# Performance work log

Hardware: AMD Instinct MI355X
Metric: run time of the kernel (lower is better)

The kernel has to match this reference:

```python
import jax, jax.numpy as jnp
import numpy as np

V = 8192        # num_embeddings == n_nodes
E = 262144      # n_edges (avg degree 32)
N = 262144      # lookup batch
D = 128         # out_channels
LAMDA = 0.8
EPS = 1e-12


def setup_inputs() -> dict:
    key = jax.random.key(0)
    k0, k1, k2, k3, k4 = jax.random.split(key, 5)
    x = jax.random.randint(k0, (N,), 0, V)
    edge_index = jax.random.randint(k1, (2, E), 0, V)
    edge_weight = jax.random.uniform(k2, (E,), dtype=jnp.float32)
    embedding = jax.random.normal(k3, (V, V), dtype=jnp.float32) * 0.02
    W = jax.random.normal(k4, (V, D), dtype=jnp.float32) * (1.0 / np.sqrt(V))
    b = jnp.zeros((D,), dtype=jnp.float32)
    return {"x": x, "edge_index": edge_index, "edge_weight": edge_weight,
            "embedding": embedding, "W": W, "b": b}


def reference(x, edge_index, edge_weight, embedding, W, b):
    # Embedding_sim: linear transform then sparse adjacency propagation
    H = embedding @ W + b                       # [V, D]
    src, dst = edge_index[0], edge_index[1]
    msg = H[src] * edge_weight[:, None]         # gather + weight, [E, D]
    P = jax.ops.segment_sum(msg, dst, num_segments=V)  # spmm(A, H), [V, D]
    emb = LAMDA * P + (1.0 - LAMDA) * H         # [V, D]
    # dropout is identity in eval mode
    out = emb[x]                                # embedding lookup, [N, D]
    norm = jnp.linalg.norm(out, axis=-1, keepdims=True)
    return out / jnp.maximum(norm, EPS)         # F.normalize (L2, dim=1)
```

## Files before the change

kernel.cpp:

```cpp
#include <hip/hip_runtime.h>
#include <hip/hip_bf16.h>

#define V     8192
#define E_N   262144
#define NN    262144
#define D     128
#define KDIM  8192

typedef __attribute__((ext_vector_type(8))) short b16x8;
typedef __attribute__((ext_vector_type(8))) unsigned short u16x8;
typedef __attribute__((ext_vector_type(4))) float f32x4;
typedef __attribute__((ext_vector_type(4))) unsigned int u32x4;

static __device__ __forceinline__ unsigned short f2bf(float f) {
    union { float f; unsigned int u; } v; v.f = f;
    unsigned int r = v.u + 0x7FFFu + ((v.u >> 16) & 1u);
    return (unsigned short)(r >> 16);
}

__global__ void k_wbt(const float* __restrict__ W, unsigned short* __restrict__ WbT) {
    __shared__ float tile[32][33];
    int bk = blockIdx.x & 255;
    int bn = blockIdx.x >> 8;
    int r = threadIdx.x >> 5;
    int c = threadIdx.x & 31;
    int k0 = bk * 32, n0 = bn * 32;
    for (int i = 0; i < 4; i++)
        tile[r + 8 * i][c] = W[(size_t)(k0 + r + 8 * i) * D + n0 + c];
    __syncthreads();
    for (int i = 0; i < 4; i++)
        WbT[(size_t)(n0 + r + 8 * i) * KDIM + k0 + c] = f2bf(tile[c][r + 8 * i]);
}

__global__ void k_initH(float* __restrict__ H, const float* __restrict__ b) {
    int t = blockIdx.x * 256 + threadIdx.x;
    H[t] = b[t & (D - 1)];
}

__global__ void k_hist(const int* __restrict__ dst, int* __restrict__ hist) {
    int e = blockIdx.x * 256 + threadIdx.x;
    if (e < E_N) atomicAdd(&hist[dst[e]], 1);
}

__global__ void k_scan(const int* __restrict__ hist, int* __restrict__ offsets,
                       int* __restrict__ cursor) {
    __shared__ int part[1024];
    int t = threadIdx.x;
    int base = t * 8;
    int loc[8]; int s = 0;
    for (int i = 0; i < 8; i++) { loc[i] = s; s += hist[base + i]; }
    part[t] = s;
    __syncthreads();
    for (int st = 1; st < 1024; st <<= 1) {
        int v = (t >= st) ? part[t - st] : 0;
        __syncthreads();
        part[t] += v;
        __syncthreads();
    }
    int ex = (t == 0) ? 0 : part[t - 1];
    for (int i = 0; i < 8; i++) {
        int o = ex + loc[i];
        offsets[base + i] = o;
        cursor[base + i] = o;
    }
    if (t == 1023) offsets[8192] = ex + s;
}

__global__ void k_scatter(const int* __restrict__ srcI, const int* __restrict__ dstI,
                          const float* __restrict__ w, int* __restrict__ cursor,
                          int* __restrict__ src_s, float* __restrict__ w_s) {
    int e = blockIdx.x * 256 + threadIdx.x;
    if (e < E_N) {
        int dnode = dstI[e];
        int pos = atomicAdd(&cursor[dnode], 1);
        src_s[pos] = srcI[e];
        w_s[pos]  = w[e];
    }
}

__global__ void __launch_bounds__(256) k_gemm(const float* __restrict__ A,
                                              const unsigned short* __restrict__ WbT,
                                              float* __restrict__ H) {
    __shared__ unsigned short As[64][72];
    __shared__ unsigned short Bs[128][72];

    int rb = blockIdx.x >> 2;
    int ks = blockIdx.x & 3;
    int tid = threadIdx.x;
    int wave = tid >> 6, lane = tid & 63;
    int r16 = lane & 15, kg = lane >> 4;

    int arow = tid >> 2, ak0 = (tid & 3) * 16;
    int brow = tid >> 1, bk0 = (tid & 1) * 32;

    const float* aPtr = A + (size_t)(rb * 64 + arow) * KDIM + ks * 2048 + ak0;
    const unsigned short* bPtr = WbT + (size_t)brow * KDIM + ks * 2048 + bk0;

    f32x4 acc[8];
    f32x4 zero = {0.f, 0.f, 0.f, 0.f};
    for (int t = 0; t < 8; t++) acc[t] = zero;

    for (int kk = 0; kk < 32; kk++) {
        f32x4 av[4];
        u32x4 bv[4];
        #pragma unroll
        for (int i = 0; i < 4; i++) av[i] = *(const f32x4*)(aPtr + i * 4);
        #pragma unroll
        for (int i = 0; i < 4; i++) bv[i] = *(const u32x4*)(bPtr + i * 8);
        aPtr += 64; bPtr += 64;

        __syncthreads();
        u16x8 p0, p1;
        #pragma unroll
        for (int j = 0; j < 4; j++) {
            p0[j]     = f2bf(av[0][j]);  p0[j + 4] = f2bf(av[1][j]);
            p1[j]     = f2bf(av[2][j]);  p1[j + 4] = f2bf(av[3][j]);
        }
        *(u16x8*)&As[arow][ak0]     = p0;
        *(u16x8*)&As[arow][ak0 + 8] = p1;
        #pragma unroll
        for (int i = 0; i < 4; i++) *(u32x4*)&Bs[brow][bk0 + i * 8] = bv[i];
        __syncthreads();

        #pragma unroll
        for (int s = 0; s < 2; s++) {
            b16x8 af = *(const b16x8*)&As[wave * 16 + r16][s * 32 + kg * 8];
            #pragma unroll
            for (int t = 0; t < 8; t++) {
                b16x8 bf = *(const b16x8*)&Bs[t * 16 + r16][s * 32 + kg * 8];
                acc[t] = __builtin_amdgcn_mfma_f32_16x16x32_bf16(af, bf, acc[t], 0, 0, 0);
            }
        }
    }

    int rbase = rb * 64 + wave * 16 + kg * 4;
    #pragma unroll
    for (int t = 0; t < 8; t++) {
        int col = t * 16 + r16;
        #pragma unroll
        for (int j = 0; j < 4; j++)
            atomicAdd(&H[(size_t)(rbase + j) * D + col], acc[t][j]);
    }
}

__global__ void k_emb(const float* __restrict__ H, const int* __restrict__ offsets,
                      const int* __restrict__ src_s, const float* __restrict__ w_s,
                      float* __restrict__ embn) {
    __shared__ float red[128];
    int v = blockIdx.x;
    int d = threadIdx.x;
    int s0 = offsets[v], s1 = offsets[v + 1];
    float acc = 0.f;
    for (int i = s0; i < s1; i++) {
        int s = src_s[i];
        float w = w_s[i];
        acc = fmaf(w, H[(size_t)s * D + d], acc);
    }
    float e = 0.8f * acc + 0.2f * H[(size_t)v * D + d];
    red[d] = e * e;
    __syncthreads();
    for (int st = 64; st > 0; st >>= 1) {
        if (d < st) red[d] += red[d + st];
        __syncthreads();
    }
    float norm = sqrtf(red[0]);
    float scale = 1.f / fmaxf(norm, 1e-12f);
    embn[(size_t)v * D + d] = e * scale;
}

__global__ void k_out(const int* __restrict__ x, const float* __restrict__ embn,
                      float* __restrict__ out) {
    int t = blockIdx.x * 256 + threadIdx.x;
    int n = t >> 5, c = t & 31;
    int xv = x[n];
    ((f32x4*)out)[t] = ((const f32x4*)embn)[xv * 32 + c];
}

extern "C" void kernel_launch(void* const* d_in, const int* in_sizes, int n_in,
                              void* d_out, int out_size, void* d_ws, size_t ws_size,
                              hipStream_t stream) {
    const int*   x      = (const int*)d_in[0];
    const int*   eSrc   = (const int*)d_in[1];
    const int*   eDst   = ((const int*)d_in[1]) + E_N;
    const float* eW     = (const float*)d_in[2];
    const float* A      = (const float*)d_in[3];
    const float* W      = (const float*)d_in[4];
    const float* b      = (const float*)d_in[5];
    float* out = (float*)d_out;

    char* ws = (char*)d_ws;
    unsigned short* WbT = (unsigned short*)(ws);
    float* H            = (float*)(ws + (2u << 20));
    float* embn         = (float*)(ws + (6u << 20));
    int* offsets        = (int*)(ws + (10u << 20));
    int* cursor         = (int*)(ws + (10u << 20) + 40960);
    int* src_s          = (int*)(ws + (10u << 20) + 131072);
    float* w_s          = (float*)(ws + (10u << 20) + 131072 + (1u << 20));

    hipMemsetAsync(cursor, 0, V * sizeof(int), stream);
    k_wbt    <<<1024, 256, 0, stream>>>(W, WbT);
    k_initH  <<<(V * D) / 256, 256, 0, stream>>>(H, b);
    k_hist   <<<E_N / 256, 256, 0, stream>>>(eDst, cursor);
    k_scan   <<<1, 1024, 0, stream>>>(cursor, offsets, cursor);
    k_scatter<<<E_N / 256, 256, 0, stream>>>(eSrc, eDst, eW, cursor, src_s, w_s);
    k_gemm   <<<512, 256, 0, stream>>>(A, WbT, H);
    k_emb    <<<V, D, 0, stream>>>(H, offsets, src_s, w_s, embn);
    k_out    <<<(NN * 32) / 256, 256, 0, stream>>>(x, embn, out);
}
```

Baseline: 201.6 us.

## Restructure GEMM with async global-to-LDS A staging and direct B register loads

The GEMM kernel now stages fp32 A tiles straight into double-buffered LDS with global_load_lds and waits only on vmcnt instead of block barriers. B fragments are loaded directly from global into registers rather than through shared memory. A is converted with the packed bf16 convert instruction, and the K split grows from 4 to 8 with twice as many blocks. The goal is to overlap the 256MB A stream with MFMA work and drop the barrier and LDS round trips. The costs are more atomic adds into H and reliance on hand-counted waitcnt values, which could be fragile.

```diff
diff --git a/kernel.cpp b/kernel.cpp
--- a/kernel.cpp
+++ b/kernel.cpp
@@ -8,14 +8,18 @@
 #define KDIM  8192
 
 typedef __attribute__((ext_vector_type(8))) short b16x8;
-typedef __attribute__((ext_vector_type(8))) unsigned short u16x8;
 typedef __attribute__((ext_vector_type(4))) float f32x4;
-typedef __attribute__((ext_vector_type(4))) unsigned int u32x4;
 
 static __device__ __forceinline__ unsigned short f2bf(float f) {
     union { float f; unsigned int u; } v; v.f = f;
     unsigned int r = v.u + 0x7FFFu + ((v.u >> 16) & 1u);
     return (unsigned short)(r >> 16);
+}
+
+static __device__ __forceinline__ unsigned int cvtpk(float lo, float hi) {
+    unsigned int r;
+    asm("v_cvt_pk_bf16_f32 %0, %1, %2" : "=v"(r) : "v"(lo), "v"(hi));
+    return r;
 }
 
 __global__ void k_wbt(const float* __restrict__ W, unsigned short* __restrict__ WbT) {
@@ -81,59 +85,67 @@
 __global__ void __launch_bounds__(256) k_gemm(const float* __restrict__ A,
                                               const unsigned short* __restrict__ WbT,
                                               float* __restrict__ H) {
-    __shared__ unsigned short As[64][72];
-    __shared__ unsigned short Bs[128][72];
-
-    int rb = blockIdx.x >> 2;
-    int ks = blockIdx.x & 3;
-    int tid = threadIdx.x;
-    int wave = tid >> 6, lane = tid & 63;
-    int r16 = lane & 15, kg = lane >> 4;
-
-    int arow = tid >> 2, ak0 = (tid & 3) * 16;
-    int brow = tid >> 1, bk0 = (tid & 1) * 32;
-
-    const float* aPtr = A + (size_t)(rb * 64 + arow) * KDIM + ks * 2048 + ak0;
-    const unsigned short* bPtr = WbT + (size_t)brow * KDIM + ks * 2048 + bk0;
+    __shared__ float Asl[2][64][32];
+
+    const int rb   = blockIdx.x >> 3;
+    const int ks   = blockIdx.x & 7;
+    const int tid  = threadIdx.x;
+    const int w    = tid >> 6;
+    const int lane = tid & 63;
+    const int r16  = lane & 15;
+    const int kg   = lane >> 4;
+
+    const float* aSrc0 = A + (size_t)(rb * 64 + w * 16 + (lane >> 3)) * KDIM
+                           + ks * 1024 + (lane & 7) * 4;
+    const float* aSrc1 = aSrc0 + (size_t)8 * KDIM;
+
+    const unsigned short* bBase = WbT + (size_t)r16 * KDIM + ks * 1024 + kg * 8;
 
     f32x4 acc[8];
     f32x4 zero = {0.f, 0.f, 0.f, 0.f};
+    #pragma unroll
     for (int t = 0; t < 8; t++) acc[t] = zero;
 
-    for (int kk = 0; kk < 32; kk++) {
-        f32x4 av[4];
-        u32x4 bv[4];
+#define STAGE(nk, nb)                                                                  \
+    do {                                                                               \
+        __builtin_amdgcn_global_load_lds(                                              \
+            (const __attribute__((address_space(1))) void*)(aSrc0 + (nk) * 32),        \
+            (__attribute__((address_space(3))) void*)&Asl[nb][w * 16][0], 16, 0, 0);   \
+        __builtin_amdgcn_global_load_lds(                                              \
+            (const __attribute__((address_space(1))) void*)(aSrc1 + (nk) * 32),        \
+            (__attribute__((address_space(3))) void*)&Asl[nb][w * 16 + 8][0], 16, 0, 0);\
+    } while (0)
+
+    STAGE(0, 0);
+
+    for (int kt = 0; kt < 32; ++kt) {
+        b16x8 bv[8];
         #pragma unroll
-        for (int i = 0; i < 4; i++) av[i] = *(const f32x4*)(aPtr + i * 4);
+        for (int t = 0; t < 8; t++)
+            bv[t] = *(const b16x8*)(bBase + (size_t)t * 16 * KDIM + kt * 32);
+
+        asm volatile("s_waitcnt lgkmcnt(0)" ::: "memory");
+        const int nk = (kt + 1 < 32) ? kt + 1 : 31;
+        STAGE(nk, (kt + 1) & 1);
+
+        asm volatile("s_waitcnt vmcnt(10)" ::: "memory");
+
+        const float* ap = &Asl[kt & 1][w * 16 + r16][kg * 8];
+        f32x4 a0 = *(const f32x4*)ap;
+        f32x4 a1 = *(const f32x4*)(ap + 4);
+        union { b16x8 v; unsigned int u[4]; } af;
+        af.u[0] = cvtpk(a0[0], a0[1]);
+        af.u[1] = cvtpk(a0[2], a0[3]);
+        af.u[2] = cvtpk(a1[0], a1[1]);
+        af.u[3] = cvtpk(a1[2], a1[3]);
+
         #pragma unroll
-        for (int i = 0; i < 4; i++) bv[i] = *(const u32x4*)(bPtr + i * 8);
-        aPtr += 64; bPtr += 64;
-
-        __syncthreads();
-        u16x8 p0, p1;
-        #pragma unroll
-        for (int j = 0; j < 4; j++) {
-            p0[j]     = f2bf(av[0][j]);  p0[j + 4] = f2bf(av[1][j]);
-            p1[j]     = f2bf(av[2][j]);  p1[j + 4] = f2bf(av[3][j]);
-        }
-        *(u16x8*)&As[arow][ak0]     = p0;
-        *(u16x8*)&As[arow][ak0 + 8] = p1;
-        #pragma unroll
-        for (int i = 0; i < 4; i++) *(u32x4*)&Bs[brow][bk0 + i * 8] = bv[i];
-        __syncthreads();
-
-        #pragma unroll
-        for (int s = 0; s < 2; s++) {
-            b16x8 af = *(const b16x8*)&As[wave * 16 + r16][s * 32 + kg * 8];
-            #pragma unroll
-            for (int t = 0; t < 8; t++) {
-                b16x8 bf = *(const b16x8*)&Bs[t * 16 + r16][s * 32 + kg * 8];
-                acc[t] = __builtin_amdgcn_mfma_f32_16x16x32_bf16(af, bf, acc[t], 0, 0, 0);
-            }
-        }
-    }
-
-    int rbase = rb * 64 + wave * 16 + kg * 4;
+        for (int t = 0; t < 8; t++)
+            acc[t] = __builtin_amdgcn_mfma_f32_16x16x32_bf16(af.v, bv[t], acc[t], 0, 0, 0);
+    }
+#undef STAGE
+
+    const int rbase = rb * 64 + w * 16 + kg * 4;
     #pragma unroll
     for (int t = 0; t < 8; t++) {
         int col = t * 16 + r16;
@@ -203,7 +215,7 @@
     k_hist   <<<E_N / 256, 256, 0, stream>>>(eDst, cursor);
     k_scan   <<<1, 1024, 0, stream>>>(cursor, offsets, cursor);
     k_scatter<<<E_N / 256, 256, 0, stream>>>(eSrc, eDst, eW, cursor, src_s, w_s);
-    k_gemm   <<<512, 256, 0, stream>>>(A, WbT, H);
+    k_gemm   <<<1024, 256, 0, stream>>>(A, WbT, H);
     k_emb    <<<V, D, 0, stream>>>(H, offsets, src_s, w_s, embn);
     k_out    <<<(NN * 32) / 256, 256, 0, stream>>>(x, embn, out);
 }
```

After: 268.5 us. 33.2% more time.
